# Kernel optimization log

Measured on AMD Instinct MI355X. Metric: run time of the kernel, lower is better.

## Reference

```python
import jax, jax.numpy as jnp
import numpy as np

N, IN_F, OUT_F = 2048, 512, 512

def setup_inputs() -> dict:
    key = jax.random.key(0)
    kx, ka, kb = jax.random.split(key, 3)
    x = jax.random.uniform(kx, (N, IN_F), dtype=jnp.float32)          # inputs in [0,1]
    a = jax.random.uniform(ka, (OUT_F, IN_F), dtype=jnp.float32)      # weight in [0,1]
    b = jax.random.uniform(kb, (OUT_F,), dtype=jnp.float32)           # bias in [0,1]
    return {"x": x, "a": a, "b": b}

def reference(x, a, b):
    # Lukasiewicz / max-plus 'matmul':
    # y[n,o] = max(0, max_i(x[n,i] + a[o,i] - 1)), then max with bias b[o].
    inter = x[:, None, :] + a[None, :, :] - 1.0        # [N, out, in]
    y = jnp.maximum(jnp.max(inter, axis=-1), 0.0)      # [N, out]
    y = jnp.maximum(y, b[None, :])
    return y
```

## Files before the change

### kernel.cpp

```cpp
#include <hip/hip_runtime.h>
#include <cstdint>


#define NROW 2048
#define NK   512
#define NCOL 512
#define RPB  16
#define CBL  128
#define KQ   16
typedef float f32x4 __attribute__((ext_vector_type(4)));

__device__ __forceinline__ void async_load16(const float* g, float* l) {
  __builtin_amdgcn_global_load_lds(
      (const __attribute__((address_space(1))) void*)g,
      (__attribute__((address_space(3))) void*)l, 16, 0, 0);
}

__global__ __launch_bounds__(256) void luka_prep(const float* __restrict__ A,
                                                 f32x4* __restrict__ Apb) {
  int idx = blockIdx.x * 256 + threadIdx.x;
  int o  = idx >> 7;
  int k4 = idx & 127;
  f32x4 v = *(const f32x4*)(A + o * NK + k4 * 4);
  Apb[(((o >> 7) * 128) + k4) * 128 + (o & 127)] = v;
}

__global__ __launch_bounds__(512, 4) void luka_main(
    const f32x4* __restrict__ Apb, const float* __restrict__ X,
    const float* __restrict__ Bv, float* __restrict__ Y) {
  __shared__ float lds[RPB * NK];
  const int tid  = threadIdx.x;
  const int lane = tid & 63;
  const int w    = tid >> 6;
  const int colblk  = blockIdx.x;
  const int rowBase = blockIdx.y * RPB;

  {
    const float* Xg = X + (size_t)rowBase * NK;
#pragma unroll
    for (int rnd = 0; rnd < 4; ++rnd) {
      int base = rnd * 512 + w * 64;
      async_load16(Xg + (size_t)(base + lane) * 4, &lds[base * 4]);
    }
  }

  const f32x4* __restrict__ Aw =
      Apb + ((size_t)(colblk * 128 + w * KQ) * 128 + lane);

  float acc[RPB][2];
#pragma unroll
  for (int r = 0; r < RPB; ++r) { acc[r][0] = 0.0f; acc[r][1] = 0.0f; }

  __syncthreads();

#pragma unroll 4
  for (int j = 0; j < KQ; ++j) {
    const f32x4 a0 = Aw[j * 128];
    const f32x4 a1 = Aw[j * 128 + 64];
    const int kb = (w * KQ + j) * 4;
#pragma unroll
    for (int r = 0; r < RPB; ++r) {
      const f32x4 xv = *(const f32x4*)&lds[r * NK + kb];
      f32x4 s0 = a0 + xv;
      f32x4 s1 = a1 + xv;
      acc[r][0] = fmaxf(fmaxf(s0.x, s0.y), acc[r][0]);
      acc[r][0] = fmaxf(fmaxf(s0.z, s0.w), acc[r][0]);
      acc[r][1] = fmaxf(fmaxf(s1.x, s1.y), acc[r][1]);
      acc[r][1] = fmaxf(fmaxf(s1.z, s1.w), acc[r][1]);
    }
  }

  const float bv = Bv[colblk * CBL + (tid & 127)];
  __syncthreads();
#pragma unroll 1
  for (int half = 0; half < 2; ++half) {
#pragma unroll
    for (int r = 0; r < 8; ++r) {
      lds[(w * 8 + r) * CBL + lane]      = acc[half * 8 + r][0];
      lds[(w * 8 + r) * CBL + 64 + lane] = acc[half * 8 + r][1];
    }
    __syncthreads();
#pragma unroll
    for (int e0 = 0; e0 < 2; ++e0) {
      int e   = e0 * 512 + tid;
      int row = e >> 7, col = e & 127;
      float m = lds[row * CBL + col];
#pragma unroll
      for (int ww = 1; ww < 8; ++ww)
        m = fmaxf(m, lds[(ww * 8 + row) * CBL + col]);
      float t = m - 1.0f;
      Y[(size_t)(rowBase + half * 8 + row) * NCOL + colblk * CBL + col] =
          fmaxf(fmaxf(t, bv), 0.0f);
    }
    __syncthreads();
  }
}

#define TILE 64
#define BK   64
__global__ __launch_bounds__(256) void luka_fb(
    const float* __restrict__ X, const float* __restrict__ A,
    const float* __restrict__ Bv, float* __restrict__ Y) {
  __shared__ float xs[2][TILE * BK];
  __shared__ float as[2][TILE * BK];
  const int tid = threadIdx.x, wave = tid >> 6, tx = tid & 15, ty = tid >> 4;
  const int rowBase = blockIdx.y * TILE, colBase = blockIdx.x * TILE;
  uint32_t xoff[4], aoff[4];
#pragma unroll
  for (int r = 0; r < 4; ++r) {
    int row = ty * 4 + r;
    xoff[r] = (uint32_t)row * 256u + ((uint32_t)((row & 15) ^ (row >> 2)) << 4);
  }
#pragma unroll
  for (int c = 0; c < 4; ++c) {
    int row = tx * 4 + c;
    aoff[c] = (uint32_t)row * 256u + ((uint32_t)((row & 15) ^ (row >> 2)) << 4);
  }
  float acc[4][4];
#pragma unroll
  for (int r = 0; r < 4; ++r)
#pragma unroll
    for (int c = 0; c < 4; ++c) acc[r][c] = 0.0f;
  const int row0 = tid >> 4, sl = tid & 15;
  auto stage = [&](int buf, int kt) {
#pragma unroll
    for (int j = 0; j < 4; ++j) {
      int row = row0 + j * 16;
      int m = (row & 15) ^ (row >> 2);
      int kk = ((sl ^ m) << 2);
      async_load16(X + (size_t)(rowBase + row) * NK + kt * BK + kk,
                   &xs[buf][j * 1024 + wave * 256]);
      async_load16(A + (size_t)(colBase + row) * NK + kt * BK + kk,
                   &as[buf][j * 1024 + wave * 256]);
    }
  };
  stage(0, 0);
  __syncthreads();
  int buf = 0;
#pragma unroll 1
  for (int kt = 0; kt < NK / BK; ++kt) {
    if (kt < NK / BK - 1) stage(buf ^ 1, kt + 1);
    const char* xb = (const char*)&xs[buf][0];
    const char* ab = (const char*)&as[buf][0];
#pragma unroll
    for (int s4 = 0; s4 < BK / 4; ++s4) {
      f32x4 xf[4], af[4];
#pragma unroll
      for (int r = 0; r < 4; ++r)
        xf[r] = *(const f32x4*)(xb + (xoff[r] ^ (uint32_t)(s4 << 4)));
#pragma unroll
      for (int c = 0; c < 4; ++c)
        af[c] = *(const f32x4*)(ab + (aoff[c] ^ (uint32_t)(s4 << 4)));
#pragma unroll
      for (int r = 0; r < 4; ++r)
#pragma unroll
        for (int c = 0; c < 4; ++c) {
          f32x4 s = xf[r] + af[c];
          float t0 = fmaxf(fmaxf(s.x, s.y), acc[r][c]);
          acc[r][c] = fmaxf(fmaxf(s.z, s.w), t0);
        }
    }
    __syncthreads();
    buf ^= 1;
  }
  const f32x4 bv = *(const f32x4*)&Bv[colBase + tx * 4];
  float bvv[4] = {bv.x, bv.y, bv.z, bv.w};
#pragma unroll
  for (int r = 0; r < 4; ++r) {
    f32x4 o;
    o.x = fmaxf(fmaxf(acc[r][0] - 1.0f, bvv[0]), 0.0f);
    o.y = fmaxf(fmaxf(acc[r][1] - 1.0f, bvv[1]), 0.0f);
    o.z = fmaxf(fmaxf(acc[r][2] - 1.0f, bvv[2]), 0.0f);
    o.w = fmaxf(fmaxf(acc[r][3] - 1.0f, bvv[3]), 0.0f);
    *(f32x4*)&Y[(size_t)(rowBase + ty * 4 + r) * NCOL + colBase + tx * 4] = o;
  }
}

extern "C" void kernel_launch(void* const* d_in, const int* in_sizes, int n_in,
                              void* d_out, int out_size, void* d_ws, size_t ws_size,
                              hipStream_t stream) {
  const float* X = (const float*)d_in[0];
  const float* A = (const float*)d_in[1];
  const float* B = (const float*)d_in[2];
  float* Y = (float*)d_out;

  if (ws_size >= (size_t)NCOL * NK * sizeof(float)) {
    f32x4* Apb = (f32x4*)d_ws;
    luka_prep<<<dim3(NCOL * NK / 4 / 256), dim3(256), 0, stream>>>(A, Apb);
    dim3 grid(NCOL / CBL, NROW / RPB);
    luka_main<<<grid, dim3(512), 0, stream>>>(Apb, X, B, Y);
  } else {
    dim3 grid(NCOL / TILE, NROW / TILE);
    luka_fb<<<grid, dim3(256), 0, stream>>>(X, A, B, Y);
  }
}
```

Measured before the change: 84.45 us.

## Widen column block to 256 with 1024-thread blocks and register-prefetched A

The column tile doubles to 256 so each thread now holds four f32x4 weight vectors and sixteen rows, which raises reuse of each LDS x read. Blocks grow to 1024 threads with a shorter per-wave K slice. The A loads are software-prefetched one step ahead in registers. The cross-wave reduction moves to a separate shared buffer and runs in four passes of four rows over 16 waves. The risks are higher register pressure, a bigger LDS footprint (32KB + 64KB) that may cut occupancy, and half as many blocks in the grid.

```diff
diff --git a/kernel.cpp b/kernel.cpp
--- a/kernel.cpp
+++ b/kernel.cpp
@@ -6,8 +6,8 @@
 #define NK   512
 #define NCOL 512
 #define RPB  16
-#define CBL  128
-#define KQ   16
+#define CBL  256
+#define KQ   8
 typedef float f32x4 __attribute__((ext_vector_type(4)));
 
 __device__ __forceinline__ void async_load16(const float* g, float* l) {
@@ -22,13 +22,14 @@
   int o  = idx >> 7;
   int k4 = idx & 127;
   f32x4 v = *(const f32x4*)(A + o * NK + k4 * 4);
-  Apb[(((o >> 7) * 128) + k4) * 128 + (o & 127)] = v;
-}
-
-__global__ __launch_bounds__(512, 4) void luka_main(
+  Apb[(((o >> 8) * 128) + k4) * 256 + (o & 255)] = v;
+}
+
+__global__ __launch_bounds__(1024, 4) void luka_main(
     const f32x4* __restrict__ Apb, const float* __restrict__ X,
     const float* __restrict__ Bv, float* __restrict__ Y) {
   __shared__ float lds[RPB * NK];
+  __shared__ float red[16 * 4 * CBL];
   const int tid  = threadIdx.x;
   const int lane = tid & 63;
   const int w    = tid >> 6;
@@ -38,60 +39,66 @@
   {
     const float* Xg = X + (size_t)rowBase * NK;
 #pragma unroll
-    for (int rnd = 0; rnd < 4; ++rnd) {
-      int base = rnd * 512 + w * 64;
+    for (int rnd = 0; rnd < 2; ++rnd) {
+      int base = rnd * 1024 + w * 64;
       async_load16(Xg + (size_t)(base + lane) * 4, &lds[base * 4]);
     }
   }
 
   const f32x4* __restrict__ Aw =
-      Apb + ((size_t)(colblk * 128 + w * KQ) * 128 + lane);
-
-  float acc[RPB][2];
-#pragma unroll
-  for (int r = 0; r < RPB; ++r) { acc[r][0] = 0.0f; acc[r][1] = 0.0f; }
+      Apb + ((size_t)(colblk * 128 + w * KQ) * 256 + lane);
+
+  float acc[RPB][4];
+#pragma unroll
+  for (int r = 0; r < RPB; ++r)
+#pragma unroll
+    for (int c = 0; c < 4; ++c) acc[r][c] = 0.0f;
+
+  f32x4 a[4], an[4];
+#pragma unroll
+  for (int c = 0; c < 4; ++c) a[c] = Aw[c * 64];
 
   __syncthreads();
 
-#pragma unroll 4
+#pragma unroll
   for (int j = 0; j < KQ; ++j) {
-    const f32x4 a0 = Aw[j * 128];
-    const f32x4 a1 = Aw[j * 128 + 64];
+    if (j + 1 < KQ) {
+#pragma unroll
+      for (int c = 0; c < 4; ++c) an[c] = Aw[(j + 1) * 256 + c * 64];
+    }
     const int kb = (w * KQ + j) * 4;
 #pragma unroll
     for (int r = 0; r < RPB; ++r) {
       const f32x4 xv = *(const f32x4*)&lds[r * NK + kb];
-      f32x4 s0 = a0 + xv;
-      f32x4 s1 = a1 + xv;
-      acc[r][0] = fmaxf(fmaxf(s0.x, s0.y), acc[r][0]);
-      acc[r][0] = fmaxf(fmaxf(s0.z, s0.w), acc[r][0]);
-      acc[r][1] = fmaxf(fmaxf(s1.x, s1.y), acc[r][1]);
-      acc[r][1] = fmaxf(fmaxf(s1.z, s1.w), acc[r][1]);
-    }
-  }
-
-  const float bv = Bv[colblk * CBL + (tid & 127)];
-  __syncthreads();
+#pragma unroll
+      for (int c = 0; c < 4; ++c) {
+        f32x4 s = a[c] + xv;
+        acc[r][c] = fmaxf(fmaxf(s.x, s.y), acc[r][c]);
+        acc[r][c] = fmaxf(fmaxf(s.z, s.w), acc[r][c]);
+      }
+    }
+#pragma unroll
+    for (int c = 0; c < 4; ++c) a[c] = an[c];
+  }
+
+  const int rc = tid >> 8;
+  const int cc = tid & 255;
+  const float bv = Bv[colblk * CBL + cc];
 #pragma unroll 1
-  for (int half = 0; half < 2; ++half) {
-#pragma unroll
-    for (int r = 0; r < 8; ++r) {
-      lds[(w * 8 + r) * CBL + lane]      = acc[half * 8 + r][0];
-      lds[(w * 8 + r) * CBL + 64 + lane] = acc[half * 8 + r][1];
-    }
+  for (int p = 0; p < 4; ++p) {
+#pragma unroll
+    for (int r2 = 0; r2 < 4; ++r2)
+#pragma unroll
+      for (int c = 0; c < 4; ++c)
+        red[(w * 4 + r2) * CBL + c * 64 + lane] = acc[p * 4 + r2][c];
     __syncthreads();
-#pragma unroll
-    for (int e0 = 0; e0 < 2; ++e0) {
-      int e   = e0 * 512 + tid;
-      int row = e >> 7, col = e & 127;
-      float m = lds[row * CBL + col];
-#pragma unroll
-      for (int ww = 1; ww < 8; ++ww)
-        m = fmaxf(m, lds[(ww * 8 + row) * CBL + col]);
-      float t = m - 1.0f;
-      Y[(size_t)(rowBase + half * 8 + row) * NCOL + colblk * CBL + col] =
-          fmaxf(fmaxf(t, bv), 0.0f);
-    }
+    float m = red[rc * CBL + cc];
+#pragma unroll
+    for (int ww = 1; ww < 16; ++ww)
+      m = fmaxf(m, red[(ww * 4 + rc) * CBL + cc]);
+    float t = m - 1.0f;
+    Y[(size_t)(rowBase + p * 4 + rc) * NCOL + colblk * CBL + cc] =
+        fmaxf(fmaxf(t, bv), 0.0f);
     __syncthreads();
   }
 }
@@ -188,7 +195,7 @@
     f32x4* Apb = (f32x4*)d_ws;
     luka_prep<<<dim3(NCOL * NK / 4 / 256), dim3(256), 0, stream>>>(A, Apb);
     dim3 grid(NCOL / CBL, NROW / RPB);
-    luka_main<<<grid, dim3(512), 0, stream>>>(Apb, X, B, Y);
+    luka_main<<<grid, dim3(1024), 0, stream>>>(Apb, X, B, Y);
   } else {
     dim3 grid(NCOL / TILE, NROW / TILE);
     luka_fb<<<grid, dim3(256), 0, stream>>>(X, A, B, Y);
```

New measurement: 146.0 us. +72.9%, slower.
